# Kernel tuning notes

Hardware: AMD Instinct MI355X
Metric: run time of the kernel (lower is better)

## Reference

```python
import jax, jax.numpy as jnp
import numpy as np

NAT, NN = 10000, 32
RSN, THETAN, NEMB = 16, 8, 4
RC = 5.0
ZETA = 16.0
FEAT = RSN * NEMB + RSN * THETAN * NEMB  # 576
PI = 3.141592653589793


def setup_inputs() -> dict:
    key = jax.random.key(0)
    ks = jax.random.split(key, 12)
    positions = jax.random.normal(ks[0], (NAT, 3), dtype=jnp.float32) * 2.0
    species_encoder = jax.random.normal(ks[1], (NAT, NEMB), dtype=jnp.float32)
    theta_s = jax.random.uniform(ks[2], (THETAN,), dtype=jnp.float32) * PI
    kn_rad = jnp.ones((1,), dtype=jnp.float32)
    neighbor_idx = jax.random.randint(ks[3], (NAT, NN), 0, NAT, dtype=jnp.int32)
    W1 = jax.random.normal(ks[4], (FEAT, 64), dtype=jnp.float32) / np.sqrt(FEAT)
    b1 = jnp.zeros((64,), dtype=jnp.float32)
    W2 = jax.random.normal(ks[5], (64, 64), dtype=jnp.float32) / 8.0
    b2 = jnp.zeros((64,), dtype=jnp.float32)
    W3 = jax.random.normal(ks[6], (64, 1), dtype=jnp.float32) / 8.0
    b3 = jnp.zeros((1,), dtype=jnp.float32)
    return {"positions": positions, "species_encoder": species_encoder,
            "theta_s": theta_s, "kn_rad": kn_rad,
            "W1": W1, "b1": b1, "W2": W2, "b2": b2, "W3": W3, "b3": b3,
            "neighbor_idx": neighbor_idx}


def _bessel_radial(rnorm, kn_rad):
    # spherical-Bessel radial basis with smooth cosine cutoff (help_fn.bessel_function)
    fc = 0.5 * (jnp.cos(PI * rnorm / RC) + 1.0) * (rnorm < RC).astype(rnorm.dtype)
    k = jnp.arange(1, RSN + 1, dtype=rnorm.dtype)                     # [RSN]
    arg = (PI / RC) * kn_rad[0] * k[None, None, :] * rnorm[..., None]  # [nat,NN,RSN]
    return jnp.sqrt(2.0 / RC) * jnp.sin(arg) / rnorm[..., None] * fc[..., None]


def reference(positions, species_encoder, theta_s, kn_rad,
              W1, b1, W2, b2, W3, b3, neighbor_idx):
    # gather neighbor displacements: [nat, NN, 3]
    rij = positions[neighbor_idx] - positions[:, None, :]
    rnorm = jnp.linalg.norm(rij, axis=-1) + 1e-8                      # [nat, NN]

    bf = _bessel_radial(rnorm, kn_rad)                                # [nat, NN, RSN]
    # center-x-neighbor species embedding product (einsum 'ijk->ik->ijk')
    semb_ij = species_encoder[neighbor_idx] * species_encoder[:, None, :]  # [nat,NN,NEMB]

    # radial descriptors: [nat, RSN, NEMB] -> [nat, RSN*NEMB]
    desc_rad = jnp.einsum('ijl,ijm->ilm', bf, semb_ij).reshape(NAT, -1)

    # angular part
    rij_unit = rij / rnorm[..., None]
    cos_ijk = jnp.einsum('ijc,ikc->ijk', rij_unit, rij_unit)          # [nat,NN,NN]
    cos_ijk = jnp.clip(cos_ijk, -1.0 + 1e-6, 1.0 - 1e-6)
    sin_ijk = jnp.sqrt(1.0 - cos_ijk * cos_ijk)
    ct, st = jnp.cos(theta_s), jnp.sin(theta_s)

    # factorized per-bond channel tensor P: [nat, NN, RSN*NEMB]
    P = jnp.einsum('ijl,ijm->ijlm', bf, semb_ij).reshape(NAT, NN, RSN * NEMB)
    pref = 2.0 ** (1.0 - ZETA)
    ang = []
    for t in range(THETAN):  # small fixed loop over angle centers
        cosd = cos_ijk * ct[t] + sin_ijk * st[t]                      # cos(theta - theta_s)
        A = pref * (1.0 + cosd) ** ZETA                               # [nat,NN,NN]
        C = jnp.einsum('ijk,ijp->ikp', A, P)                          # contract over j
        ang.append(jnp.sum(C * P, axis=1))                            # [nat, RSN*NEMB]
    desc_ang = jnp.stack(ang, axis=1).reshape(NAT, -1)                # [nat, THETAN*RSN*NEMB]

    desc = jnp.concatenate([desc_rad, desc_ang], axis=1)              # [nat, FEAT]

    # per-atom MLP -> atomic energies, scatter-sum to total energy
    h = jnp.tanh(desc @ W1 + b1)
    h = jnp.tanh(h @ W2 + b2)
    e_atom = (h @ W3 + b3)[:, 0]                                      # [nat]
    return jnp.sum(e_atom)
```

## Files before the change

### kernel.cpp

```cpp
#include <hip/hip_runtime.h>
#include <hip/hip_bf16.h>

#define NATC 10000
#define NATP 10016
#define NNC 32
#define RSNC 16
#define THETANC 8
#define NEMBC 4
#define FEATC 576

typedef __attribute__((ext_vector_type(8))) short short8;
typedef __attribute__((ext_vector_type(4))) float f32x4;

static __device__ __forceinline__ short f2bf(float x) {
    union { __hip_bfloat16 h; short s; } u;
    u.h = __float2bfloat16(x);
    return u.s;
}

__global__ __launch_bounds__(256) void prep_kernel(
    const float* __restrict__ W1, const float* __restrict__ W2,
    ushort* __restrict__ W1p, ushort* __restrict__ W2p)
{
    const int gid = blockIdx.x * 256 + threadIdx.x;
    if (gid < 4608) {
        const int l = gid & 63, ntks = gid >> 6;
        const int nt = ntks & 3, ks = ntks >> 2;
        const int q = l >> 4, c = l & 15;
        ushort pk[8];
        #pragma unroll
        for (int jj = 0; jj < 8; ++jj)
            pk[jj] = (ushort)f2bf(W1[(ks * 32 + q * 8 + jj) * 64 + nt * 16 + c]);
        #pragma unroll
        for (int jj = 0; jj < 8; ++jj) W1p[gid * 8 + jj] = pk[jj];
    } else {
        const int g = gid - 4608;
        const int l = g & 63, ntks = g >> 6;
        const int nt = ntks & 3, ks = ntks >> 2;
        const int q = l >> 4, c = l & 15;
        ushort pk[8];
        #pragma unroll
        for (int jj = 0; jj < 8; ++jj)
            pk[jj] = (ushort)f2bf(W2[(ks * 32 + q * 8 + jj) * 64 + nt * 16 + c]);
        #pragma unroll
        for (int jj = 0; jj < 8; ++jj) W2p[g * 8 + jj] = pk[jj];
    }
}

__global__ __launch_bounds__(256, 4) void desc_kernel(
    const float* __restrict__ pos,
    const float* __restrict__ spe,
    const float* __restrict__ theta_s,
    const float* __restrict__ kn_rad,
    const int* __restrict__ nidx,
    ushort* __restrict__ descb)
{
    constexpr float RC = 5.0f;
    constexpr float PI_F = 3.14159265358979323846f;
    constexpr float PREF = 3.0517578125e-05f;

    __shared__ __attribute__((aligned(16))) float ux[NNC], uy[NNC], uz[NNC];
    __shared__ __attribute__((aligned(16))) float rbase[NNC], rw[NNC];
    __shared__ __attribute__((aligned(16))) float bfs[NNC * 17];
    __shared__ __attribute__((aligned(16))) float ses[NNC * 5];
    __shared__ __attribute__((aligned(16))) float P[NNC * 65];
    __shared__ __attribute__((aligned(16))) float cosm[NNC * 33];
    __shared__ __attribute__((aligned(16))) float sinm[NNC * 33];
    __shared__ __attribute__((aligned(16))) short Pb[4 * 64 * 8];

    const int i   = blockIdx.x;
    const int tid = threadIdx.x;

    if (tid < NNC) {
        const int j = tid;
        const int n = nidx[i * NNC + j];
        const float pix = pos[i * 3 + 0], piy = pos[i * 3 + 1], piz = pos[i * 3 + 2];
        const float dx = pos[n * 3 + 0] - pix;
        const float dy = pos[n * 3 + 1] - piy;
        const float dz = pos[n * 3 + 2] - piz;
        const float r = sqrtf(dx * dx + dy * dy + dz * dz) + 1e-8f;
        const float inv = 1.0f / r;
        ux[j] = dx * inv; uy[j] = dy * inv; uz[j] = dz * inv;
        const float fc = (r < RC) ? 0.5f * (cosf(PI_F * r * (1.0f / RC)) + 1.0f) : 0.0f;
        rbase[j] = sqrtf(2.0f / RC) * inv * fc;
        rw[j]    = (PI_F / RC) * kn_rad[0] * r;
        #pragma unroll
        for (int m = 0; m < NEMBC; ++m)
            ses[j * 5 + m] = spe[n * NEMBC + m] * spe[i * NEMBC + m];
    }
    __syncthreads();

    #pragma unroll
    for (int k = 0; k < 2; ++k) {
        const int e = tid + k * 256;
        const int j = e >> 4, l = e & 15;
        bfs[j * 17 + l] = rbase[j] * sinf(rw[j] * (float)(l + 1));
    }
    __syncthreads();

    #pragma unroll
    for (int k = 0; k < 8; ++k) {
        const int e = tid + k * 256;
        const int j = e >> 6, p = e & 63;
        P[j * 65 + p] = bfs[j * 17 + (p >> 2)] * ses[j * 5 + (p & 3)];
    }
    #pragma unroll
    for (int k = 0; k < 4; ++k) {
        const int idx = tid + k * 256;
        const int j = idx >> 5, kk = idx & 31;
        float c = ux[j] * ux[kk] + uy[j] * uy[kk] + uz[j] * uz[kk];
        c = fminf(fmaxf(c, -1.0f + 1e-6f), 1.0f - 1e-6f);
        cosm[j * 33 + kk] = c;
        sinm[j * 33 + kk] = sqrtf(fmaxf(1.0f - c * c, 0.0f));
    }
    __syncthreads();

    {
        const int nt = tid >> 6, l2 = tid & 63;
        const int q2 = l2 >> 4, c2 = l2 & 15;
        short8 pk;
        #pragma unroll
        for (int jj = 0; jj < 8; ++jj)
            pk[jj] = f2bf(P[(q2 * 8 + jj) * 65 + nt * 16 + c2]);
        *(short8*)&Pb[(nt * 64 + l2) * 8] = pk;
    }
    if (tid < 64) {
        float s = 0.0f;
        #pragma unroll 8
        for (int j = 0; j < NNC; ++j) s += P[j * 65 + tid];
        descb[(size_t)i * FEATC + tid] = (ushort)f2bf(s);
    }
    __syncthreads();

    const int w = tid >> 6, l = tid & 63;
    const int q = l >> 4, c = l & 15;

    for (int tt = 0; tt < 2; ++tt) {
        const int t = w + tt * 4;
        const float th = theta_s[t];
        const float ct = cosf(th), st = sinf(th);

        short8 afr[2];
        #pragma unroll
        for (int mt = 0; mt < 2; ++mt) {
            const int kk = mt * 16 + c;
            #pragma unroll
            for (int jj = 0; jj < 8; ++jj) {
                const int j = q * 8 + jj;
                const float cv = cosm[kk * 33 + j];
                const float sv = sinm[kk * 33 + j];
                const float cosd = fmaf(cv, ct, sv * st);
                const float x = 1.0f + cosd;
                const float x2 = x * x, x4 = x2 * x2, x8 = x4 * x4;
                afr[mt][jj] = f2bf(PREF * (x8 * x8));
            }
        }

        f32x4 acc[2][4];
        #pragma unroll
        for (int mt = 0; mt < 2; ++mt)
            #pragma unroll
            for (int nt = 0; nt < 4; ++nt)
                acc[mt][nt] = (f32x4){0.0f, 0.0f, 0.0f, 0.0f};

        #pragma unroll
        for (int nt = 0; nt < 4; ++nt) {
            const short8 bfr = *(const short8*)&Pb[(nt * 64 + l) * 8];
            acc[0][nt] = __builtin_amdgcn_mfma_f32_16x16x32_bf16(afr[0], bfr, acc[0][nt], 0, 0, 0);
            acc[1][nt] = __builtin_amdgcn_mfma_f32_16x16x32_bf16(afr[1], bfr, acc[1][nt], 0, 0, 0);
        }

        float pt[4];
        #pragma unroll
        for (int nt = 0; nt < 4; ++nt) {
            float s = 0.0f;
            #pragma unroll
            for (int mt = 0; mt < 2; ++mt)
                #pragma unroll
                for (int r = 0; r < 4; ++r) {
                    const int kk = mt * 16 + q * 4 + r;
                    s = fmaf(acc[mt][nt][r], P[kk * 65 + nt * 16 + c], s);
                }
            s += __shfl_xor(s, 16, 64);
            s += __shfl_xor(s, 32, 64);
            pt[nt] = s;
        }
        const float v = (q == 0) ? pt[0] : (q == 1) ? pt[1] : (q == 2) ? pt[2] : pt[3];
        descb[(size_t)i * FEATC + 64 + t * 64 + l] = (ushort)f2bf(v);
    }
}

__global__ __launch_bounds__(256) void mlp_kernel(
    const ushort* __restrict__ descb,
    const ushort* __restrict__ W1p, const float* __restrict__ b1,
    const ushort* __restrict__ W2p, const float* __restrict__ b2,
    const float* __restrict__ W3, const float* __restrict__ b3,
    float* __restrict__ out)
{
    __shared__ __attribute__((aligned(16))) ushort H1b[32 * 72];
    __shared__ float red[4];

    const int tid = threadIdx.x;
    const int w = tid >> 6, l = tid & 63;
    const int q = l >> 4, c = l & 15;
    const int a0 = blockIdx.x * 32;

    f32x4 acc[2];
    acc[0] = (f32x4){0.0f, 0.0f, 0.0f, 0.0f};
    acc[1] = (f32x4){0.0f, 0.0f, 0.0f, 0.0f};

    #pragma unroll 3
    for (int ks = 0; ks < 18; ++ks) {
        const short8 b = *(const short8*)&W1p[((ks * 4 + w) * 64 + l) * 8];
        #pragma unroll
        for (int mt = 0; mt < 2; ++mt) {
            const int a = a0 + mt * 16 + c;
            const short8 afr = *(const short8*)&descb[(size_t)a * FEATC + ks * 32 + q * 8];
            acc[mt] = __builtin_amdgcn_mfma_f32_16x16x32_bf16(afr, b, acc[mt], 0, 0, 0);
        }
    }

    const float b1v = b1[w * 16 + c];
    #pragma unroll
    for (int mt = 0; mt < 2; ++mt)
        #pragma unroll
        for (int r = 0; r < 4; ++r) {
            const int m = mt * 16 + q * 4 + r;
            H1b[m * 72 + w * 16 + c] = (ushort)f2bf(tanhf(acc[mt][r] + b1v));
        }
    __syncthreads();

    f32x4 acc2[2];
    acc2[0] = (f32x4){0.0f, 0.0f, 0.0f, 0.0f};
    acc2[1] = (f32x4){0.0f, 0.0f, 0.0f, 0.0f};
    #pragma unroll
    for (int ks = 0; ks < 2; ++ks) {
        const short8 b = *(const short8*)&W2p[((ks * 4 + w) * 64 + l) * 8];
        #pragma unroll
        for (int mt = 0; mt < 2; ++mt) {
            const short8 afr = *(const short8*)&H1b[(mt * 16 + c) * 72 + ks * 32 + q * 8];
            acc2[mt] = __builtin_amdgcn_mfma_f32_16x16x32_bf16(afr, b, acc2[mt], 0, 0, 0);
        }
    }

    const float b2v = b2[w * 16 + c];
    const float w3v = W3[w * 16 + c];
    float s = 0.0f;
    #pragma unroll
    for (int mt = 0; mt < 2; ++mt)
        #pragma unroll
        for (int r = 0; r < 4; ++r) {
            const int a = a0 + mt * 16 + q * 4 + r;
            const float e = tanhf(acc2[mt][r] + b2v) * w3v;
            if (a < NATC) s += e;
        }
    #pragma unroll
    for (int off = 1; off <= 32; off <<= 1)
        s += __shfl_xor(s, off, 64);
    if (l == 0) red[w] = s;
    __syncthreads();
    if (tid == 0) {
        float tot = red[0] + red[1] + red[2] + red[3];
        if (blockIdx.x == 0) tot += (float)NATC * b3[0];
        atomicAdd(out, tot);
    }
}

extern "C" void kernel_launch(void* const* d_in, const int* in_sizes, int n_in,
                              void* d_out, int out_size, void* d_ws, size_t ws_size,
                              hipStream_t stream)
{
    const float* pos   = (const float*)d_in[0];
    const float* spe   = (const float*)d_in[1];
    const float* theta = (const float*)d_in[2];
    const float* kn    = (const float*)d_in[3];
    const float* W1    = (const float*)d_in[4];
    const float* b1    = (const float*)d_in[5];
    const float* W2    = (const float*)d_in[6];
    const float* b2    = (const float*)d_in[7];
    const float* W3    = (const float*)d_in[8];
    const float* b3    = (const float*)d_in[9];
    const int*   nidx  = (const int*)d_in[10];
    float* out = (float*)d_out;

    ushort* descb = (ushort*)d_ws;
    ushort* W1p   = (ushort*)((char*)d_ws + (size_t)NATP * FEATC * 2);
    ushort* W2p   = W1p + 4608 * 8;

    hipMemsetAsync(out, 0, sizeof(float), stream);
    prep_kernel<<<20, 256, 0, stream>>>(W1, W2, W1p, W2p);
    desc_kernel<<<NATC, 256, 0, stream>>>(pos, spe, theta, kn, nidx, descb);
    mlp_kernel<<<(NATC + 31) / 32, 256, 0, stream>>>(descb, W1p, b1, W2p, b2, W3, b3, out);
}
```

Before: 154.4 us.

## Shrink desc_kernel LDS footprint, vectorize LDS access, and halve MLP tile

The descriptor kernel now keeps P transposed as float4 rows and stores the cos/sin pairs interleaved. It aliases the scratch buffers into one 4 KB union to cut LDS use, and raises launch bounds from 4 to 7 blocks per CU. The angular power term folds the 2^(1-zeta) prefactor into a precomputed per-theta scale, so the per-element prefactor multiply and the per-wave theta trig calls go away. The MLP kernel processes 16 atoms per block instead of 32 to launch more blocks, and the b3 init moves into prep_kernel, replacing the memset. The risks are register pressure under the tighter launch bound and the extra MLP blocks each reloading the weights.

New measurement: 134.4 us. 1.15x faster.

```diff
diff --git a/kernel.cpp b/kernel.cpp
--- a/kernel.cpp
+++ b/kernel.cpp
@@ -11,6 +11,7 @@
 
 typedef __attribute__((ext_vector_type(8))) short short8;
 typedef __attribute__((ext_vector_type(4))) float f32x4;
+typedef __attribute__((ext_vector_type(2))) float f32x2;
 
 static __device__ __forceinline__ short f2bf(float x) {
     union { __hip_bfloat16 h; short s; } u;
@@ -20,9 +21,12 @@
 
 __global__ __launch_bounds__(256) void prep_kernel(
     const float* __restrict__ W1, const float* __restrict__ W2,
-    ushort* __restrict__ W1p, ushort* __restrict__ W2p)
+    const float* __restrict__ b3,
+    ushort* __restrict__ W1p, ushort* __restrict__ W2p,
+    float* __restrict__ out)
 {
     const int gid = blockIdx.x * 256 + threadIdx.x;
+    if (gid == 0) out[0] = (float)NATC * b3[0];
     if (gid < 4608) {
         const int l = gid & 63, ntks = gid >> 6;
         const int nt = ntks & 3, ks = ntks >> 2;
@@ -47,7 +51,7 @@
     }
 }
 
-__global__ __launch_bounds__(256, 4) void desc_kernel(
+__global__ __launch_bounds__(256, 7) void desc_kernel(
     const float* __restrict__ pos,
     const float* __restrict__ spe,
     const float* __restrict__ theta_s,
@@ -57,16 +61,22 @@
 {
     constexpr float RC = 5.0f;
     constexpr float PI_F = 3.14159265358979323846f;
-    constexpr float PREF = 3.0517578125e-05f;
-
-    __shared__ __attribute__((aligned(16))) float ux[NNC], uy[NNC], uz[NNC];
-    __shared__ __attribute__((aligned(16))) float rbase[NNC], rw[NNC];
-    __shared__ __attribute__((aligned(16))) float bfs[NNC * 17];
-    __shared__ __attribute__((aligned(16))) float ses[NNC * 5];
-    __shared__ __attribute__((aligned(16))) float P[NNC * 65];
-    __shared__ __attribute__((aligned(16))) float cosm[NNC * 33];
-    __shared__ __attribute__((aligned(16))) float sinm[NNC * 33];
-    __shared__ __attribute__((aligned(16))) short Pb[4 * 64 * 8];
+    constexpr float SF = 0.52213689121f;
+
+    __shared__ f32x4 Pt4[64 * 9];
+    __shared__ f32x4 cs4[32 * 17];
+    __shared__ float thc[16];
+    __shared__ __attribute__((aligned(16))) char uni[4096];
+
+    float* const Pt    = (float*)Pt4;
+    float* const ux    = (float*)uni;
+    float* const uy    = ux + 32;
+    float* const uz    = ux + 64;
+    float* const rbase = ux + 96;
+    float* const rw    = ux + 128;
+    float* const bfs   = ux + 160;
+    float* const ses   = ux + 704;
+    short* const Pb    = (short*)uni;
 
     const int i   = blockIdx.x;
     const int tid = threadIdx.x;
@@ -87,6 +97,11 @@
         #pragma unroll
         for (int m = 0; m < NEMBC; ++m)
             ses[j * 5 + m] = spe[n * NEMBC + m] * spe[i * NEMBC + m];
+    } else if (tid >= 64 && tid < 72) {
+        const int t = tid - 64;
+        const float th = theta_s[t];
+        thc[2 * t]     = SF * cosf(th);
+        thc[2 * t + 1] = SF * sinf(th);
     }
     __syncthreads();
 
@@ -101,33 +116,40 @@
     #pragma unroll
     for (int k = 0; k < 8; ++k) {
         const int e = tid + k * 256;
-        const int j = e >> 6, p = e & 63;
-        P[j * 65 + p] = bfs[j * 17 + (p >> 2)] * ses[j * 5 + (p & 3)];
+        const int j = e & 31, p = e >> 5;
+        Pt[p * 36 + j] = bfs[j * 17 + (p >> 2)] * ses[j * 5 + (p & 3)];
     }
     #pragma unroll
     for (int k = 0; k < 4; ++k) {
-        const int idx = tid + k * 256;
-        const int j = idx >> 5, kk = idx & 31;
-        float c = ux[j] * ux[kk] + uy[j] * uy[kk] + uz[j] * uz[kk];
-        c = fminf(fmaxf(c, -1.0f + 1e-6f), 1.0f - 1e-6f);
-        cosm[j * 33 + kk] = c;
-        sinm[j * 33 + kk] = sqrtf(fmaxf(1.0f - c * c, 0.0f));
+        const int e = tid + k * 256;
+        const int kk = e & 31, j = e >> 5;
+        float cv = ux[j] * ux[kk] + uy[j] * uy[kk] + uz[j] * uz[kk];
+        cv = fminf(fmaxf(cv, -1.0f + 1e-6f), 1.0f - 1e-6f);
+        f32x2 csv;
+        csv[0] = cv;
+        csv[1] = sqrtf(fmaxf(1.0f - cv * cv, 0.0f));
+        ((f32x2*)cs4)[kk * 34 + j] = csv;
     }
     __syncthreads();
 
     {
         const int nt = tid >> 6, l2 = tid & 63;
         const int q2 = l2 >> 4, c2 = l2 & 15;
+        const f32x4 x0 = Pt4[(nt * 16 + c2) * 9 + q2 * 2];
+        const f32x4 x1 = Pt4[(nt * 16 + c2) * 9 + q2 * 2 + 1];
         short8 pk;
-        #pragma unroll
-        for (int jj = 0; jj < 8; ++jj)
-            pk[jj] = f2bf(P[(q2 * 8 + jj) * 65 + nt * 16 + c2]);
-        *(short8*)&Pb[(nt * 64 + l2) * 8] = pk;
+        pk[0] = f2bf(x0[0]); pk[1] = f2bf(x0[1]); pk[2] = f2bf(x0[2]); pk[3] = f2bf(x0[3]);
+        pk[4] = f2bf(x1[0]); pk[5] = f2bf(x1[1]); pk[6] = f2bf(x1[2]); pk[7] = f2bf(x1[3]);
+        *(short8*)&Pb[tid * 8] = pk;
     }
     if (tid < 64) {
+        const f32x4* pr = &Pt4[tid * 9];
         float s = 0.0f;
-        #pragma unroll 8
-        for (int j = 0; j < NNC; ++j) s += P[j * 65 + tid];
+        #pragma unroll
+        for (int kb = 0; kb < 8; ++kb) {
+            const f32x4 v = pr[kb];
+            s += v[0]; s += v[1]; s += v[2]; s += v[3];
+        }
         descb[(size_t)i * FEATC + tid] = (ushort)f2bf(s);
     }
     __syncthreads();
@@ -135,24 +157,24 @@
     const int w = tid >> 6, l = tid & 63;
     const int q = l >> 4, c = l & 15;
 
+    #pragma unroll
     for (int tt = 0; tt < 2; ++tt) {
         const int t = w + tt * 4;
-        const float th = theta_s[t];
-        const float ct = cosf(th), st = sinf(th);
+        const float tc = thc[2 * t], ts = thc[2 * t + 1];
 
         short8 afr[2];
         #pragma unroll
         for (int mt = 0; mt < 2; ++mt) {
             const int kk = mt * 16 + c;
+            const f32x4* crow = &cs4[kk * 17 + q * 4];
+            const f32x4 vv[4] = { crow[0], crow[1], crow[2], crow[3] };
             #pragma unroll
             for (int jj = 0; jj < 8; ++jj) {
-                const int j = q * 8 + jj;
-                const float cv = cosm[kk * 33 + j];
-                const float sv = sinm[kk * 33 + j];
-                const float cosd = fmaf(cv, ct, sv * st);
-                const float x = 1.0f + cosd;
-                const float x2 = x * x, x4 = x2 * x2, x8 = x4 * x4;
-                afr[mt][jj] = f2bf(PREF * (x8 * x8));
+                const float cv = vv[jj >> 1][(jj & 1) * 2];
+                const float sv = vv[jj >> 1][(jj & 1) * 2 + 1];
+                const float y  = fmaf(cv, tc, fmaf(sv, ts, SF));
+                const float y2 = y * y, y4 = y2 * y2, y8 = y4 * y4;
+                afr[mt][jj] = f2bf(y8 * y8);
             }
         }
 
@@ -170,22 +192,22 @@
             acc[1][nt] = __builtin_amdgcn_mfma_f32_16x16x32_bf16(afr[1], bfr, acc[1][nt], 0, 0, 0);
         }
 
-        float pt[4];
+        float ptv[4];
         #pragma unroll
         for (int nt = 0; nt < 4; ++nt) {
             float s = 0.0f;
             #pragma unroll
-            for (int mt = 0; mt < 2; ++mt)
+            for (int mt = 0; mt < 2; ++mt) {
+                const f32x4 pv = Pt4[(nt * 16 + c) * 9 + mt * 4 + q];
                 #pragma unroll
-                for (int r = 0; r < 4; ++r) {
-                    const int kk = mt * 16 + q * 4 + r;
-                    s = fmaf(acc[mt][nt][r], P[kk * 65 + nt * 16 + c], s);
-                }
+                for (int r = 0; r < 4; ++r)
+                    s = fmaf(acc[mt][nt][r], pv[r], s);
+            }
             s += __shfl_xor(s, 16, 64);
             s += __shfl_xor(s, 32, 64);
-            pt[nt] = s;
-        }
-        const float v = (q == 0) ? pt[0] : (q == 1) ? pt[1] : (q == 2) ? pt[2] : pt[3];
+            ptv[nt] = s;
+        }
+        const float v = (q == 0) ? ptv[0] : (q == 1) ? ptv[1] : (q == 2) ? ptv[2] : ptv[3];
         descb[(size_t)i * FEATC + 64 + t * 64 + l] = (ushort)f2bf(v);
     }
 }
@@ -194,76 +216,55 @@
     const ushort* __restrict__ descb,
     const ushort* __restrict__ W1p, const float* __restrict__ b1,
     const ushort* __restrict__ W2p, const float* __restrict__ b2,
-    const float* __restrict__ W3, const float* __restrict__ b3,
+    const float* __restrict__ W3,
     float* __restrict__ out)
 {
-    __shared__ __attribute__((aligned(16))) ushort H1b[32 * 72];
+    __shared__ __attribute__((aligned(16))) ushort H1b[16 * 72];
     __shared__ float red[4];
 
     const int tid = threadIdx.x;
     const int w = tid >> 6, l = tid & 63;
     const int q = l >> 4, c = l & 15;
-    const int a0 = blockIdx.x * 32;
-
-    f32x4 acc[2];
-    acc[0] = (f32x4){0.0f, 0.0f, 0.0f, 0.0f};
-    acc[1] = (f32x4){0.0f, 0.0f, 0.0f, 0.0f};
-
-    #pragma unroll 3
+    const int a0 = blockIdx.x * 16;
+
+    f32x4 acc = (f32x4){0.0f, 0.0f, 0.0f, 0.0f};
+
+    #pragma unroll 6
     for (int ks = 0; ks < 18; ++ks) {
-        const short8 b = *(const short8*)&W1p[((ks * 4 + w) * 64 + l) * 8];
-        #pragma unroll
-        for (int mt = 0; mt < 2; ++mt) {
-            const int a = a0 + mt * 16 + c;
-            const short8 afr = *(const short8*)&descb[(size_t)a * FEATC + ks * 32 + q * 8];
-            acc[mt] = __builtin_amdgcn_mfma_f32_16x16x32_bf16(afr, b, acc[mt], 0, 0, 0);
-        }
+        const short8 b   = *(const short8*)&W1p[((ks * 4 + w) * 64 + l) * 8];
+        const short8 afr = *(const short8*)&descb[(size_t)(a0 + c) * FEATC + ks * 32 + q * 8];
+        acc = __builtin_amdgcn_mfma_f32_16x16x32_bf16(afr, b, acc, 0, 0, 0);
     }
 
     const float b1v = b1[w * 16 + c];
     #pragma unroll
-    for (int mt = 0; mt < 2; ++mt)
-        #pragma unroll
-        for (int r = 0; r < 4; ++r) {
-            const int m = mt * 16 + q * 4 + r;
-            H1b[m * 72 + w * 16 + c] = (ushort)f2bf(tanhf(acc[mt][r] + b1v));
-        }
-    __syncthreads();
-
-    f32x4 acc2[2];
-    acc2[0] = (f32x4){0.0f, 0.0f, 0.0f, 0.0f};
-    acc2[1] = (f32x4){0.0f, 0.0f, 0.0f, 0.0f};
+    for (int r = 0; r < 4; ++r)
+        H1b[(q * 4 + r) * 72 + w * 16 + c] = (ushort)f2bf(tanhf(acc[r] + b1v));
+    __syncthreads();
+
+    f32x4 acc2 = (f32x4){0.0f, 0.0f, 0.0f, 0.0f};
     #pragma unroll
     for (int ks = 0; ks < 2; ++ks) {
-        const short8 b = *(const short8*)&W2p[((ks * 4 + w) * 64 + l) * 8];
-        #pragma unroll
-        for (int mt = 0; mt < 2; ++mt) {
-            const short8 afr = *(const short8*)&H1b[(mt * 16 + c) * 72 + ks * 32 + q * 8];
-            acc2[mt] = __builtin_amdgcn_mfma_f32_16x16x32_bf16(afr, b, acc2[mt], 0, 0, 0);
-        }
+        const short8 b   = *(const short8*)&W2p[((ks * 4 + w) * 64 + l) * 8];
+        const short8 afr = *(const short8*)&H1b[c * 72 + ks * 32 + q * 8];
+        acc2 = __builtin_amdgcn_mfma_f32_16x16x32_bf16(afr, b, acc2, 0, 0, 0);
     }
 
     const float b2v = b2[w * 16 + c];
     const float w3v = W3[w * 16 + c];
     float s = 0.0f;
     #pragma unroll
-    for (int mt = 0; mt < 2; ++mt)
-        #pragma unroll
-        for (int r = 0; r < 4; ++r) {
-            const int a = a0 + mt * 16 + q * 4 + r;
-            const float e = tanhf(acc2[mt][r] + b2v) * w3v;
-            if (a < NATC) s += e;
-        }
+    for (int r = 0; r < 4; ++r) {
+        const int a = a0 + q * 4 + r;
+        if (a < NATC) s += tanhf(acc2[r] + b2v) * w3v;
+    }
     #pragma unroll
     for (int off = 1; off <= 32; off <<= 1)
         s += __shfl_xor(s, off, 64);
     if (l == 0) red[w] = s;
     __syncthreads();
-    if (tid == 0) {
-        float tot = red[0] + red[1] + red[2] + red[3];
-        if (blockIdx.x == 0) tot += (float)NATC * b3[0];
-        atomicAdd(out, tot);
-    }
+    if (tid == 0)
+        atomicAdd(out, red[0] + red[1] + red[2] + red[3]);
 }
 
 extern "C" void kernel_launch(void* const* d_in, const int* in_sizes, int n_in,
@@ -287,8 +288,7 @@
     ushort* W1p   = (ushort*)((char*)d_ws + (size_t)NATP * FEATC * 2);
     ushort* W2p   = W1p + 4608 * 8;
 
-    hipMemsetAsync(out, 0, sizeof(float), stream);
-    prep_kernel<<<20, 256, 0, stream>>>(W1, W2, W1p, W2p);
+    prep_kernel<<<20, 256, 0, stream>>>(W1, W2, b3, W1p, W2p, out);
     desc_kernel<<<NATC, 256, 0, stream>>>(pos, spe, theta, kn, nidx, descb);
-    mlp_kernel<<<(NATC + 31) / 32, 256, 0, stream>>>(descb, W1p, b1, W2p, b2, W3, b3, out);
-}
+    mlp_kernel<<<(NATC + 15) / 16, 256, 0, stream>>>(descb, W1p, b1, W2p, b2, W3, out);
+}
```
